# Performance work log

Measured on AMD Instinct MI355X. Metric: run time of the kernel, lower is better.

The kernel has to match this reference:

```python
import jax, jax.numpy as jnp
import numpy as np

SIGMA = 32.0
MAGNITUDE = 1.0


def setup_inputs() -> dict:
    key = jax.random.key(0)
    k1, k2, k3 = jax.random.split(key, 3)
    N = 512
    W = 2048
    L = 2048
    init_vectors = jax.random.normal(k1, (2, N), dtype=jnp.float32)
    x_coord = jax.random.randint(k2, (N,), 0, W)
    y_coord = jax.random.randint(k3, (N,), 0, L)
    return {
        "init_vectors": init_vectors,
        "x_coord": x_coord,
        "y_coord": y_coord,
        "width": W,
        "lenth": L,
    }


def reference(init_vectors, x_coord, y_coord, width, lenth):
    # Scale vectors exactly as the torch module: randn / ((lenth+width)/32) * magnitude
    v = init_vectors * (MAGNITUDE / ((lenth + width) / 32.0))  # [2, N]
    inv2s2 = 1.0 / (2.0 * SIGMA * SIGMA)
    xs = jnp.arange(width, dtype=jnp.float32)   # [W]
    ys = jnp.arange(lenth, dtype=jnp.float32)   # [L]
    xc = x_coord.astype(jnp.float32)            # [N]
    yc = y_coord.astype(jnp.float32)            # [N]
    # Gaussian is separable: exp(-(dx^2+dy^2)/2s^2) = exp(-dx^2/2s^2)*exp(-dy^2/2s^2)
    wx = jnp.exp(-((xs[:, None] - xc[None, :]) ** 2) * inv2s2)  # [W, N]
    wy = jnp.exp(-((ys[:, None] - yc[None, :]) ** 2) * inv2s2)  # [L, N]
    # field[c,x,y] = sum_n wx[x,n] * wy[y,n] * v[c,n]
    t = jnp.einsum("xn,cn->cxn", wx, v)          # [2, W, N] (small)
    field = jnp.einsum("cxn,yn->cxy", t, wy)     # [2, W, L]
    return field[None]                            # [1, 2, W, L]
```

## Files before the change

### kernel.cpp

```cpp
#include <hip/hip_runtime.h>
#include <math.h>


#define N_MAX  512
#define TX     32
#define TY     64
#define R_CUT  112.0f

#define EXP2F(x) __builtin_amdgcn_exp2f(x)

typedef float f4 __attribute__((ext_vector_type(4)));

__global__ __launch_bounds__(256, 8) void motion_field_kernel(
    const float* __restrict__ init_vectors,
    const int*   __restrict__ x_coord,
    const int*   __restrict__ y_coord,
    const int*   __restrict__ d_width,
    const int*   __restrict__ d_lenth,
    float*       __restrict__ out,
    int N, int W, int L)
{
    __shared__ float2 s_xy[N_MAX];
    __shared__ float2 s_v[N_MAX];
    __shared__ short  s_list[N_MAX];
    __shared__ int    s_cnt[4];
    __shared__ float  s_w[4][2][64];

    const int tid  = threadIdx.x;
    const int wave = tid >> 6;
    const int lane = tid & 63;

    const float S = 0.02654008814f;
    const float scale = 32.0f / (float)(d_width[0] + d_lenth[0]);

    for (int i = tid; i < N; i += 256) {
        s_xy[i] = make_float2((float)x_coord[i] * S, (float)y_coord[i] * S);
        s_v[i]  = make_float2(init_vectors[i] * scale, init_vectors[N + i] * scale);
    }
    __syncthreads();

    const int x0 = blockIdx.x * TX;
    const int y0 = blockIdx.y * TY;
    const float bx_lo = ((float)x0 - R_CUT) * S;
    const float bx_hi = ((float)(x0 + TX - 1) + R_CUT) * S;
    const float by_lo = ((float)y0 - R_CUT) * S;
    const float by_hi = ((float)(y0 + TY - 1) + R_CUT) * S;

    int total = 0;
    for (int base_n = 0; base_n < N; base_n += 256) {
        const int n = base_n + tid;
        bool pred = false;
        if (n < N) {
            const float2 xy = s_xy[n];
            pred = (xy.x >= bx_lo) && (xy.x <= bx_hi) &&
                   (xy.y >= by_lo) && (xy.y <= by_hi);
        }
        const unsigned long long m = __ballot(pred);
        if (lane == 0) s_cnt[wave] = __popcll(m);
        __syncthreads();
        const int c0 = s_cnt[0], c1 = s_cnt[1], c2 = s_cnt[2], c3 = s_cnt[3];
        int base = total;
        if (wave > 0) base += c0;
        if (wave > 1) base += c1;
        if (wave > 2) base += c2;
        if (pred) {
            const int pos = base + __popcll(m & ((1ULL << lane) - 1ULL));
            s_list[pos] = (short)n;
        }
        total += c0 + c1 + c2 + c3;
        __syncthreads();
    }
    const int M = total;

    const int wx = wave >> 1;
    const int wy = wave & 1;
    const int u  = lane >> 2;
    const int vq = lane & 3;

    const bool isx = (lane < 16);
    const int  wcoord = isx ? (x0 + wx * 16 + lane)
                            : (y0 + wy * 32 + (lane - 16));
    const float C = (float)wcoord * S;

    float acc0[8], acc1[8];
    #pragma unroll
    for (int j = 0; j < 8; ++j) { acc0[j] = 0.f; acc1[j] = 0.f; }

    float* const slab0 = &s_w[wave][0][0];
    float* const slab1 = &s_w[wave][1][0];

    for (int m = 0; m < M; ++m) {
        const int n = (int)s_list[m];
        const float2 xy = s_xy[n];
        const float2 v  = s_v[n];
        float* const slab = (m & 1) ? slab1 : slab0;

        const float sel = isx ? xy.x : xy.y;
        const float d   = C - sel;
        slab[lane] = EXP2F(-(d * d));
        asm volatile("s_waitcnt lgkmcnt(0)" ::: "memory");

        const float exu = slab[u];
        const f4 eyA = *(const f4*)&slab[16 + vq * 8];
        const f4 eyB = *(const f4*)&slab[16 + vq * 8 + 4];

        const float e0 = exu * v.x;
        const float e1 = exu * v.y;
        const float eys[8] = {eyA.x, eyA.y, eyA.z, eyA.w,
                              eyB.x, eyB.y, eyB.z, eyB.w};
        #pragma unroll
        for (int j = 0; j < 8; ++j) {
            acc0[j] = fmaf(e0, eys[j], acc0[j]);
            acc1[j] = fmaf(e1, eys[j], acc1[j]);
        }
    }

    const size_t WL = (size_t)W * (size_t)L;
    const int x  = x0 + wx * 16 + u;
    const int yb = y0 + wy * 32 + vq * 8;
    const size_t base = (size_t)x * (size_t)L + (size_t)yb;
    f4* p0 = (f4*)&out[base];
    f4* p1 = (f4*)&out[WL + base];
    __builtin_nontemporal_store((f4){acc0[0], acc0[1], acc0[2], acc0[3]}, p0);
    __builtin_nontemporal_store((f4){acc0[4], acc0[5], acc0[6], acc0[7]}, p0 + 1);
    __builtin_nontemporal_store((f4){acc1[0], acc1[1], acc1[2], acc1[3]}, p1);
    __builtin_nontemporal_store((f4){acc1[4], acc1[5], acc1[6], acc1[7]}, p1 + 1);
}

extern "C" void kernel_launch(void* const* d_in, const int* in_sizes, int n_in,
                              void* d_out, int out_size, void* d_ws, size_t ws_size,
                              hipStream_t stream) {
    const float* init_vectors = (const float*)d_in[0];
    const int*   x_coord      = (const int*)d_in[1];
    const int*   y_coord      = (const int*)d_in[2];
    const int*   d_width      = (const int*)d_in[3];
    const int*   d_lenth      = (const int*)d_in[4];
    float*       out          = (float*)d_out;

    const int N = in_sizes[1];
    const int WL = out_size / 2;
    int W = 1;
    while ((long long)W * (long long)W < (long long)WL) W <<= 1;
    const int L = WL / W;

    dim3 grid(W / TX, L / TY);
    dim3 block(256);
    hipLaunchKernelGGL(motion_field_kernel, grid, block, 0, stream,
                       init_vectors, x_coord, y_coord, d_width, d_lenth,
                       out, N, W, L);
}
```

Measured before the change: 16.55 us.

## Use 512-thread blocks with taller tiles, single-pass compaction, and prefetched list loads

Each block now covers 32x128 output with 8 waves instead of 32x64 with 4, so the per-block setup (loading all points into shared memory and compacting the in-range list) is amortized over twice as many outputs. With 512 threads the compaction runs as one ballot pass with a single barrier pair. The inner loop software-prefetches the next point's coordinates and vector from shared memory. Nontemporal stores are replaced with plain stores. The trade-off is that the larger tile yields a longer candidate list per block, adding more points each wave must process, and the code now assumes N is at most 512.

```diff
diff --git a/kernel.cpp b/kernel.cpp
--- a/kernel.cpp
+++ b/kernel.cpp
@@ -4,14 +4,14 @@
 
 #define N_MAX  512
 #define TX     32
-#define TY     64
+#define TY     128
 #define R_CUT  112.0f
 
 #define EXP2F(x) __builtin_amdgcn_exp2f(x)
 
 typedef float f4 __attribute__((ext_vector_type(4)));
 
-__global__ __launch_bounds__(256, 8) void motion_field_kernel(
+__global__ __launch_bounds__(512, 8) void motion_field_kernel(
     const float* __restrict__ init_vectors,
     const int*   __restrict__ x_coord,
     const int*   __restrict__ y_coord,
@@ -23,8 +23,8 @@
     __shared__ float2 s_xy[N_MAX];
     __shared__ float2 s_v[N_MAX];
     __shared__ short  s_list[N_MAX];
-    __shared__ int    s_cnt[4];
-    __shared__ float  s_w[4][2][64];
+    __shared__ int    s_cnt[8];
+    __shared__ float  s_w[8][2][64];
 
     const int tid  = threadIdx.x;
     const int wave = tid >> 6;
@@ -33,9 +33,10 @@
     const float S = 0.02654008814f;
     const float scale = 32.0f / (float)(d_width[0] + d_lenth[0]);
 
-    for (int i = tid; i < N; i += 256) {
-        s_xy[i] = make_float2((float)x_coord[i] * S, (float)y_coord[i] * S);
-        s_v[i]  = make_float2(init_vectors[i] * scale, init_vectors[N + i] * scale);
+    if (tid < N) {
+        s_xy[tid] = make_float2((float)x_coord[tid] * S, (float)y_coord[tid] * S);
+        s_v[tid]  = make_float2(init_vectors[tid] * scale,
+                                init_vectors[N + tid] * scale);
     }
     __syncthreads();
 
@@ -46,34 +47,31 @@
     const float by_lo = ((float)y0 - R_CUT) * S;
     const float by_hi = ((float)(y0 + TY - 1) + R_CUT) * S;
 
-    int total = 0;
-    for (int base_n = 0; base_n < N; base_n += 256) {
-        const int n = base_n + tid;
-        bool pred = false;
-        if (n < N) {
-            const float2 xy = s_xy[n];
-            pred = (xy.x >= bx_lo) && (xy.x <= bx_hi) &&
-                   (xy.y >= by_lo) && (xy.y <= by_hi);
-        }
-        const unsigned long long m = __ballot(pred);
-        if (lane == 0) s_cnt[wave] = __popcll(m);
-        __syncthreads();
-        const int c0 = s_cnt[0], c1 = s_cnt[1], c2 = s_cnt[2], c3 = s_cnt[3];
-        int base = total;
-        if (wave > 0) base += c0;
-        if (wave > 1) base += c1;
-        if (wave > 2) base += c2;
-        if (pred) {
-            const int pos = base + __popcll(m & ((1ULL << lane) - 1ULL));
-            s_list[pos] = (short)n;
-        }
-        total += c0 + c1 + c2 + c3;
-        __syncthreads();
+    bool pred = false;
+    if (tid < N) {
+        const float2 xy = s_xy[tid];
+        pred = (xy.x >= bx_lo) && (xy.x <= bx_hi) &&
+               (xy.y >= by_lo) && (xy.y <= by_hi);
+    }
+    const unsigned long long bm = __ballot(pred);
+    if (lane == 0) s_cnt[wave] = __popcll(bm);
+    __syncthreads();
+    int base = 0, total = 0;
+    #pragma unroll
+    for (int w = 0; w < 8; ++w) {
+        const int c = s_cnt[w];
+        if (w < wave) base += c;
+        total += c;
+    }
+    if (pred) {
+        const int pos = base + __popcll(bm & ((1ULL << lane) - 1ULL));
+        s_list[pos] = (short)tid;
     }
     const int M = total;
+    __syncthreads();
 
-    const int wx = wave >> 1;
-    const int wy = wave & 1;
+    const int wx = wave >> 2;
+    const int wy = wave & 3;
     const int u  = lane >> 2;
     const int vq = lane & 3;
 
@@ -89,42 +87,50 @@
     float* const slab0 = &s_w[wave][0][0];
     float* const slab1 = &s_w[wave][1][0];
 
-    for (int m = 0; m < M; ++m) {
-        const int n = (int)s_list[m];
-        const float2 xy = s_xy[n];
-        const float2 v  = s_v[n];
-        float* const slab = (m & 1) ? slab1 : slab0;
+    if (M > 0) {
+        int n0 = (int)s_list[0];
+        float2 xy_next = s_xy[n0];
+        float2 v_next  = s_v[n0];
+        for (int m = 0; m < M; ++m) {
+            const float2 xy = xy_next;
+            const float2 v  = v_next;
+            const int mn = (m + 1 < M) ? (m + 1) : (M - 1);
+            const int nn = (int)s_list[mn];
+            xy_next = s_xy[nn];
+            v_next  = s_v[nn];
 
-        const float sel = isx ? xy.x : xy.y;
-        const float d   = C - sel;
-        slab[lane] = EXP2F(-(d * d));
-        asm volatile("s_waitcnt lgkmcnt(0)" ::: "memory");
+            float* const slab = (m & 1) ? slab1 : slab0;
+            const float sel = isx ? xy.x : xy.y;
+            const float d   = C - sel;
+            slab[lane] = EXP2F(-(d * d));
+            asm volatile("s_waitcnt lgkmcnt(0)" ::: "memory");
 
-        const float exu = slab[u];
-        const f4 eyA = *(const f4*)&slab[16 + vq * 8];
-        const f4 eyB = *(const f4*)&slab[16 + vq * 8 + 4];
+            const float exu = slab[u];
+            const f4 eyA = *(const f4*)&slab[16 + vq * 8];
+            const f4 eyB = *(const f4*)&slab[16 + vq * 8 + 4];
 
-        const float e0 = exu * v.x;
-        const float e1 = exu * v.y;
-        const float eys[8] = {eyA.x, eyA.y, eyA.z, eyA.w,
-                              eyB.x, eyB.y, eyB.z, eyB.w};
-        #pragma unroll
-        for (int j = 0; j < 8; ++j) {
-            acc0[j] = fmaf(e0, eys[j], acc0[j]);
-            acc1[j] = fmaf(e1, eys[j], acc1[j]);
+            const float e0 = exu * v.x;
+            const float e1 = exu * v.y;
+            const float eys[8] = {eyA.x, eyA.y, eyA.z, eyA.w,
+                                  eyB.x, eyB.y, eyB.z, eyB.w};
+            #pragma unroll
+            for (int j = 0; j < 8; ++j) {
+                acc0[j] = fmaf(e0, eys[j], acc0[j]);
+                acc1[j] = fmaf(e1, eys[j], acc1[j]);
+            }
         }
     }
 
     const size_t WL = (size_t)W * (size_t)L;
     const int x  = x0 + wx * 16 + u;
     const int yb = y0 + wy * 32 + vq * 8;
-    const size_t base = (size_t)x * (size_t)L + (size_t)yb;
-    f4* p0 = (f4*)&out[base];
-    f4* p1 = (f4*)&out[WL + base];
-    __builtin_nontemporal_store((f4){acc0[0], acc0[1], acc0[2], acc0[3]}, p0);
-    __builtin_nontemporal_store((f4){acc0[4], acc0[5], acc0[6], acc0[7]}, p0 + 1);
-    __builtin_nontemporal_store((f4){acc1[0], acc1[1], acc1[2], acc1[3]}, p1);
-    __builtin_nontemporal_store((f4){acc1[4], acc1[5], acc1[6], acc1[7]}, p1 + 1);
+    const size_t off = (size_t)x * (size_t)L + (size_t)yb;
+    f4* p0 = (f4*)&out[off];
+    f4* p1 = (f4*)&out[WL + off];
+    p0[0] = (f4){acc0[0], acc0[1], acc0[2], acc0[3]};
+    p0[1] = (f4){acc0[4], acc0[5], acc0[6], acc0[7]};
+    p1[0] = (f4){acc1[0], acc1[1], acc1[2], acc1[3]};
+    p1[1] = (f4){acc1[4], acc1[5], acc1[6], acc1[7]};
 }
 
 extern "C" void kernel_launch(void* const* d_in, const int* in_sizes, int n_in,
@@ -144,7 +150,7 @@
     const int L = WL / W;
 
     dim3 grid(W / TX, L / TY);
-    dim3 block(256);
+    dim3 block(512);
     hipLaunchKernelGGL(motion_field_kernel, grid, block, 0, stream,
                        init_vectors, x_coord, y_coord, d_width, d_lenth,
                        out, N, W, L);
```

New measurement: 16.95 us. +2.4%, slower.

## Give each wave its own 32x32 tile with per-wave culling list and packed FMAs

Applied to the files above, without the earlier changes.

Each wave now owns an independent 32x32 output tile and builds its own list of nearby Gaussians with ballots, so the block-wide barriers in the culling phase go away. The inner loop prefetches the next source's coordinates and weights one iteration ahead. It uses all 64 lanes to compute 32 x-weights and 32 y-weights per source, and accumulates with 2-wide float vectors so the compiler can emit packed FMAs. Stores switch from nontemporal to regular, and the launch bounds drop to 4 blocks per CU, which allows more registers but may lower occupancy. The per-wave list is sized at 128 entries, so it could overflow if more than 128 sources fall within range of one tile.

```diff
diff --git a/kernel.cpp b/kernel.cpp
--- a/kernel.cpp
+++ b/kernel.cpp
@@ -3,15 +3,14 @@
 
 
 #define N_MAX  512
-#define TX     32
-#define TY     64
 #define R_CUT  112.0f
 
 #define EXP2F(x) __builtin_amdgcn_exp2f(x)
 
 typedef float f4 __attribute__((ext_vector_type(4)));
+typedef float f2 __attribute__((ext_vector_type(2)));
 
-__global__ __launch_bounds__(256, 8) void motion_field_kernel(
+__global__ __launch_bounds__(256, 4) void motion_field_kernel(
     const float* __restrict__ init_vectors,
     const int*   __restrict__ x_coord,
     const int*   __restrict__ y_coord,
@@ -22,9 +21,8 @@
 {
     __shared__ float2 s_xy[N_MAX];
     __shared__ float2 s_v[N_MAX];
-    __shared__ short  s_list[N_MAX];
-    __shared__ int    s_cnt[4];
-    __shared__ float  s_w[4][2][64];
+    __shared__ short  s_wlist[4][128];
+    __shared__ float  s_slab[4][2][64];
 
     const int tid  = threadIdx.x;
     const int wave = tid >> 6;
@@ -35,96 +33,108 @@
 
     for (int i = tid; i < N; i += 256) {
         s_xy[i] = make_float2((float)x_coord[i] * S, (float)y_coord[i] * S);
-        s_v[i]  = make_float2(init_vectors[i] * scale, init_vectors[N + i] * scale);
+        s_v[i]  = make_float2(init_vectors[i] * scale,
+                              init_vectors[N + i] * scale);
     }
     __syncthreads();
 
-    const int x0 = blockIdx.x * TX;
-    const int y0 = blockIdx.y * TY;
+    const int tilesY = L >> 5;
+    const int g  = blockIdx.x * 4 + wave;
+    const int tx = g / tilesY;
+    const int ty = g - tx * tilesY;
+    const int x0 = tx * 32;
+    const int y0 = ty * 32;
+
     const float bx_lo = ((float)x0 - R_CUT) * S;
-    const float bx_hi = ((float)(x0 + TX - 1) + R_CUT) * S;
+    const float bx_hi = ((float)(x0 + 31) + R_CUT) * S;
     const float by_lo = ((float)y0 - R_CUT) * S;
-    const float by_hi = ((float)(y0 + TY - 1) + R_CUT) * S;
+    const float by_hi = ((float)(y0 + 31) + R_CUT) * S;
 
-    int total = 0;
-    for (int base_n = 0; base_n < N; base_n += 256) {
-        const int n = base_n + tid;
+    int M = 0;
+    #pragma unroll
+    for (int r = 0; r < N_MAX / 64; ++r) {
+        const int n = r * 64 + lane;
         bool pred = false;
         if (n < N) {
             const float2 xy = s_xy[n];
             pred = (xy.x >= bx_lo) && (xy.x <= bx_hi) &&
                    (xy.y >= by_lo) && (xy.y <= by_hi);
         }
-        const unsigned long long m = __ballot(pred);
-        if (lane == 0) s_cnt[wave] = __popcll(m);
-        __syncthreads();
-        const int c0 = s_cnt[0], c1 = s_cnt[1], c2 = s_cnt[2], c3 = s_cnt[3];
-        int base = total;
-        if (wave > 0) base += c0;
-        if (wave > 1) base += c1;
-        if (wave > 2) base += c2;
+        const unsigned long long mk = __ballot(pred);
         if (pred) {
-            const int pos = base + __popcll(m & ((1ULL << lane) - 1ULL));
-            s_list[pos] = (short)n;
+            const int pos = M + (int)__popcll(mk & ((1ULL << lane) - 1ULL));
+            s_wlist[wave][pos] = (short)n;
         }
-        total += c0 + c1 + c2 + c3;
-        __syncthreads();
+        M += (int)__popcll(mk);
     }
-    const int M = total;
+    asm volatile("s_waitcnt lgkmcnt(0)" ::: "memory");
 
-    const int wx = wave >> 1;
-    const int wy = wave & 1;
+    const bool  is_ey = (lane < 32);
+    const float C = (float)(is_ey ? (y0 + lane) : (x0 + (lane - 32))) * S;
+
     const int u  = lane >> 2;
     const int vq = lane & 3;
 
-    const bool isx = (lane < 16);
-    const int  wcoord = isx ? (x0 + wx * 16 + lane)
-                            : (y0 + wy * 32 + (lane - 16));
-    const float C = (float)wcoord * S;
+    f2 acc[2][2][4];
+    #pragma unroll
+    for (int c = 0; c < 2; ++c)
+        #pragma unroll
+        for (int xi = 0; xi < 2; ++xi)
+            #pragma unroll
+            for (int p = 0; p < 4; ++p) acc[c][xi][p] = (f2){0.f, 0.f};
 
-    float acc0[8], acc1[8];
-    #pragma unroll
-    for (int j = 0; j < 8; ++j) { acc0[j] = 0.f; acc1[j] = 0.f; }
+    float* const slab0 = &s_slab[wave][0][0];
+    float* const slab1 = &s_slab[wave][1][0];
 
-    float* const slab0 = &s_w[wave][0][0];
-    float* const slab1 = &s_w[wave][1][0];
+    if (M > 0) {
+        int n0 = (int)s_wlist[wave][0];
+        float2 xy_n = s_xy[n0];
+        float2 v_n  = s_v[n0];
+        for (int m = 0; m < M; ++m) {
+            const float2 xy = xy_n;
+            const float2 v  = v_n;
+            const int mn = (m + 1 < M) ? (m + 1) : (M - 1);
+            const int nn = (int)s_wlist[wave][mn];
+            xy_n = s_xy[nn];
+            v_n  = s_v[nn];
 
-    for (int m = 0; m < M; ++m) {
-        const int n = (int)s_list[m];
-        const float2 xy = s_xy[n];
-        const float2 v  = s_v[n];
-        float* const slab = (m & 1) ? slab1 : slab0;
+            float* const slab = (m & 1) ? slab1 : slab0;
+            const float d = C - (is_ey ? xy.y : xy.x);
+            slab[lane] = EXP2F(-(d * d));
+            asm volatile("s_waitcnt lgkmcnt(0)" ::: "memory");
 
-        const float sel = isx ? xy.x : xy.y;
-        const float d   = C - sel;
-        slab[lane] = EXP2F(-(d * d));
-        asm volatile("s_waitcnt lgkmcnt(0)" ::: "memory");
+            const f2 ex2 = *(const f2*)&slab[32 + u * 2];
+            const f4 eyA = *(const f4*)&slab[vq * 8];
+            const f4 eyB = *(const f4*)&slab[vq * 8 + 4];
+            const f2 ey[4] = {(f2){eyA.x, eyA.y}, (f2){eyA.z, eyA.w},
+                              (f2){eyB.x, eyB.y}, (f2){eyB.z, eyB.w}};
 
-        const float exu = slab[u];
-        const f4 eyA = *(const f4*)&slab[16 + vq * 8];
-        const f4 eyB = *(const f4*)&slab[16 + vq * 8 + 4];
-
-        const float e0 = exu * v.x;
-        const float e1 = exu * v.y;
-        const float eys[8] = {eyA.x, eyA.y, eyA.z, eyA.w,
-                              eyB.x, eyB.y, eyB.z, eyB.w};
-        #pragma unroll
-        for (int j = 0; j < 8; ++j) {
-            acc0[j] = fmaf(e0, eys[j], acc0[j]);
-            acc1[j] = fmaf(e1, eys[j], acc1[j]);
+            const float e00 = ex2.x * v.x, e01 = ex2.y * v.x;
+            const float e10 = ex2.x * v.y, e11 = ex2.y * v.y;
+            #pragma unroll
+            for (int p = 0; p < 4; ++p) {
+                acc[0][0][p] += ey[p] * e00;
+                acc[0][1][p] += ey[p] * e01;
+                acc[1][0][p] += ey[p] * e10;
+                acc[1][1][p] += ey[p] * e11;
+            }
         }
     }
 
     const size_t WL = (size_t)W * (size_t)L;
-    const int x  = x0 + wx * 16 + u;
-    const int yb = y0 + wy * 32 + vq * 8;
-    const size_t base = (size_t)x * (size_t)L + (size_t)yb;
-    f4* p0 = (f4*)&out[base];
-    f4* p1 = (f4*)&out[WL + base];
-    __builtin_nontemporal_store((f4){acc0[0], acc0[1], acc0[2], acc0[3]}, p0);
-    __builtin_nontemporal_store((f4){acc0[4], acc0[5], acc0[6], acc0[7]}, p0 + 1);
-    __builtin_nontemporal_store((f4){acc1[0], acc1[1], acc1[2], acc1[3]}, p1);
-    __builtin_nontemporal_store((f4){acc1[4], acc1[5], acc1[6], acc1[7]}, p1 + 1);
+    const int xb = x0 + u * 2;
+    const int yb = y0 + vq * 8;
+    #pragma unroll
+    for (int c = 0; c < 2; ++c) {
+        #pragma unroll
+        for (int xi = 0; xi < 2; ++xi) {
+            float* p = &out[(size_t)c * WL + (size_t)(xb + xi) * L + (size_t)yb];
+            *(f4*)p       = (f4){acc[c][xi][0].x, acc[c][xi][0].y,
+                                 acc[c][xi][1].x, acc[c][xi][1].y};
+            *(f4*)(p + 4) = (f4){acc[c][xi][2].x, acc[c][xi][2].y,
+                                 acc[c][xi][3].x, acc[c][xi][3].y};
+        }
+    }
 }
 
 extern "C" void kernel_launch(void* const* d_in, const int* in_sizes, int n_in,
@@ -143,7 +153,8 @@
     while ((long long)W * (long long)W < (long long)WL) W <<= 1;
     const int L = WL / W;
 
-    dim3 grid(W / TX, L / TY);
+    const int tiles = (W / 32) * (L / 32);
+    dim3 grid(tiles / 4);
     dim3 block(256);
     hipLaunchKernelGGL(motion_field_kernel, grid, block, 0, stream,
                        init_vectors, x_coord, y_coord, d_width, d_lenth,
```

Measured after the change: 16.99 us. 1.03x slower.

## Retile to 16x256 blocks with batched shared-memory Gaussian weight tables

Applied to the files above, without the earlier changes.

Changes the block tile from 32x64 to 16x256 and computes x/y Gaussian weights for batches of four centers cooperatively into shared memory. Each thread then accumulates a 4x4 patch per channel using vector FMAs, replacing the per-wave per-center slab exchange. The larger y extent makes the center cull region bigger relative to the tile, and the change adds two block barriers per batch and drops to occupancy hint 4. Output stores become plain vector stores instead of nontemporal ones.

```diff
diff --git a/kernel.cpp b/kernel.cpp
--- a/kernel.cpp
+++ b/kernel.cpp
@@ -3,15 +3,16 @@
 
 
 #define N_MAX  512
-#define TX     32
-#define TY     64
+#define TX     16
+#define TY     256
 #define R_CUT  112.0f
+#define BATCH  4
 
 #define EXP2F(x) __builtin_amdgcn_exp2f(x)
 
 typedef float f4 __attribute__((ext_vector_type(4)));
 
-__global__ __launch_bounds__(256, 8) void motion_field_kernel(
+__global__ __launch_bounds__(256, 4) void motion_field_kernel(
     const float* __restrict__ init_vectors,
     const int*   __restrict__ x_coord,
     const int*   __restrict__ y_coord,
@@ -24,7 +25,8 @@
     __shared__ float2 s_v[N_MAX];
     __shared__ short  s_list[N_MAX];
     __shared__ int    s_cnt[4];
-    __shared__ float  s_w[4][2][64];
+    __shared__ float  s_ey[BATCH][TY];
+    __shared__ float  s_ex[BATCH][TX];
 
     const int tid  = threadIdx.x;
     const int wave = tid >> 6;
@@ -35,7 +37,8 @@
 
     for (int i = tid; i < N; i += 256) {
         s_xy[i] = make_float2((float)x_coord[i] * S, (float)y_coord[i] * S);
-        s_v[i]  = make_float2(init_vectors[i] * scale, init_vectors[N + i] * scale);
+        s_v[i]  = make_float2(init_vectors[i] * scale,
+                              init_vectors[N + i] * scale);
     }
     __syncthreads();
 
@@ -55,8 +58,8 @@
             pred = (xy.x >= bx_lo) && (xy.x <= bx_hi) &&
                    (xy.y >= by_lo) && (xy.y <= by_hi);
         }
-        const unsigned long long m = __ballot(pred);
-        if (lane == 0) s_cnt[wave] = __popcll(m);
+        const unsigned long long mk = __ballot(pred);
+        if (lane == 0) s_cnt[wave] = __popcll(mk);
         __syncthreads();
         const int c0 = s_cnt[0], c1 = s_cnt[1], c2 = s_cnt[2], c3 = s_cnt[3];
         int base = total;
@@ -64,7 +67,7 @@
         if (wave > 1) base += c1;
         if (wave > 2) base += c2;
         if (pred) {
-            const int pos = base + __popcll(m & ((1ULL << lane) - 1ULL));
+            const int pos = base + __popcll(mk & ((1ULL << lane) - 1ULL));
             s_list[pos] = (short)n;
         }
         total += c0 + c1 + c2 + c3;
@@ -72,59 +75,56 @@
     }
     const int M = total;
 
-    const int wx = wave >> 1;
-    const int wy = wave & 1;
-    const int u  = lane >> 2;
-    const int vq = lane & 3;
+    f4 acc[2][4];
+    #pragma unroll
+    for (int c = 0; c < 2; ++c)
+        #pragma unroll
+        for (int i = 0; i < 4; ++i) acc[c][i] = (f4){0.f, 0.f, 0.f, 0.f};
 
-    const bool isx = (lane < 16);
-    const int  wcoord = isx ? (x0 + wx * 16 + lane)
-                            : (y0 + wy * 32 + (lane - 16));
-    const float C = (float)wcoord * S;
+    const float Yl = (float)(y0 + lane * 4) * S;
 
-    float acc0[8], acc1[8];
-    #pragma unroll
-    for (int j = 0; j < 8; ++j) { acc0[j] = 0.f; acc1[j] = 0.f; }
+    for (int m0 = 0; m0 < M; m0 += BATCH) {
+        const int B = (M - m0 < BATCH) ? (M - m0) : BATCH;
 
-    float* const slab0 = &s_w[wave][0][0];
-    float* const slab1 = &s_w[wave][1][0];
+        for (int s = tid; s < B * TY; s += 256) {
+            const int b = s >> 8, y = s & (TY - 1);
+            const int n = (int)s_list[m0 + b];
+            const float dy = (float)(y0 + y) * S - s_xy[n].y;
+            s_ey[b][y] = EXP2F(-(dy * dy));
+        }
+        if (tid < B * TX) {
+            const int b = tid >> 4, r = tid & (TX - 1);
+            const int n = (int)s_list[m0 + b];
+            const float dx = (float)(x0 + r) * S - s_xy[n].x;
+            s_ex[b][r] = EXP2F(-(dx * dx));
+        }
+        __syncthreads();
 
-    for (int m = 0; m < M; ++m) {
-        const int n = (int)s_list[m];
-        const float2 xy = s_xy[n];
-        const float2 v  = s_v[n];
-        float* const slab = (m & 1) ? slab1 : slab0;
-
-        const float sel = isx ? xy.x : xy.y;
-        const float d   = C - sel;
-        slab[lane] = EXP2F(-(d * d));
-        asm volatile("s_waitcnt lgkmcnt(0)" ::: "memory");
-
-        const float exu = slab[u];
-        const f4 eyA = *(const f4*)&slab[16 + vq * 8];
-        const f4 eyB = *(const f4*)&slab[16 + vq * 8 + 4];
-
-        const float e0 = exu * v.x;
-        const float e1 = exu * v.y;
-        const float eys[8] = {eyA.x, eyA.y, eyA.z, eyA.w,
-                              eyB.x, eyB.y, eyB.z, eyB.w};
-        #pragma unroll
-        for (int j = 0; j < 8; ++j) {
-            acc0[j] = fmaf(e0, eys[j], acc0[j]);
-            acc1[j] = fmaf(e1, eys[j], acc1[j]);
+        for (int b = 0; b < B; ++b) {
+            const int n = (int)s_list[m0 + b];
+            const float2 v = s_v[n];
+            const f4 ex4 = *(const f4*)&s_ex[b][wave * 4];
+            const f4 ey4 = *(const f4*)&s_ey[b][lane * 4];
+            const float exs[4] = {ex4.x, ex4.y, ex4.z, ex4.w};
+            #pragma unroll
+            for (int i = 0; i < 4; ++i) {
+                acc[0][i] += ey4 * (exs[i] * v.x);
+                acc[1][i] += ey4 * (exs[i] * v.y);
+            }
         }
+        __syncthreads();
     }
 
     const size_t WL = (size_t)W * (size_t)L;
-    const int x  = x0 + wx * 16 + u;
-    const int yb = y0 + wy * 32 + vq * 8;
-    const size_t base = (size_t)x * (size_t)L + (size_t)yb;
-    f4* p0 = (f4*)&out[base];
-    f4* p1 = (f4*)&out[WL + base];
-    __builtin_nontemporal_store((f4){acc0[0], acc0[1], acc0[2], acc0[3]}, p0);
-    __builtin_nontemporal_store((f4){acc0[4], acc0[5], acc0[6], acc0[7]}, p0 + 1);
-    __builtin_nontemporal_store((f4){acc1[0], acc1[1], acc1[2], acc1[3]}, p1);
-    __builtin_nontemporal_store((f4){acc1[4], acc1[5], acc1[6], acc1[7]}, p1 + 1);
+    const int yb = y0 + lane * 4;
+    #pragma unroll
+    for (int c = 0; c < 2; ++c) {
+        #pragma unroll
+        for (int i = 0; i < 4; ++i) {
+            const int x = x0 + wave * 4 + i;
+            *(f4*)&out[(size_t)c * WL + (size_t)x * L + (size_t)yb] = acc[c][i];
+        }
+    }
 }
 
 extern "C" void kernel_launch(void* const* d_in, const int* in_sizes, int n_in,
```

New measurement: 17.54 us. 6.0% more time.
